# Performance work log

Measured on AMD Instinct MI355X. Metric: run time of the kernel, lower is better.

The kernel has to match this reference:

```python
import jax, jax.numpy as jnp
import numpy as np

DIM = 512; HEADS = 8; DHEAD = 64; INNER = HEADS * DHEAD
T = 9; H = 16; W = 16; KS = 5; KT = 7
SEQ = T * H * W + 1          # 2305 tokens incl. BOS
GH = 48; GW = 48             # axial grid: sqrt(T*H*W) = 48
B = 2


def _nearby_mask_np():
    """Faithful numpy port of generate_nearby_mask(causal=True). True = masked."""
    te = (KT - 1) // 2
    frame = H * W
    S = T * frame
    pad = KS // 2
    tmpl = (np.arange(KS * KS) >= (KS * KS) // 2).reshape(KS, KS)
    mb = np.ones((S, T, H + 2 * pad, W + 2 * pad), dtype=bool)
    for t in range(T):
        for h in range(H):
            for w in range(W):
                i = t * frame + h * W + w
                mb[i, t, h:h + KS, w:w + KS] = tmpl
                mb[i, max(0, t - te):t, h:h + KS, w:w + KS] = False
    mb = mb[:, :, pad:-pad, pad:-pad].reshape(S, S)
    mb = np.roll(mb, -1, axis=0)
    out = np.ones((S + 1, S + 1), dtype=bool)  # pad 1 row/col of True at top-left
    out[1:, 1:] = mb
    out[0, 0] = False
    return out


def setup_inputs() -> dict:
    key = jax.random.key(0)
    ks = jax.random.split(key, 16)
    inp = {
        "x": jax.random.normal(ks[0], (B, SEQ, DIM), jnp.float32),
        "nearby_mask": jnp.asarray(_nearby_mask_np()),
    }
    i = 1
    for l in range(3):
        for nm in ("Wq", "Wk", "Wv", "Wo"):
            inp[f"{nm}{l}"] = jax.random.normal(ks[i], (DIM, INNER), jnp.float32) * 0.02
            i += 1
        inp[f"bo{l}"] = jnp.zeros((DIM,), jnp.float32)
    return inp


def _neg(dt):
    return -jnp.finfo(dt).max


def _axial(x, Wq, Wk, Wv, Wo, bo, typ):
    # type 0: attend along rows (width axis); type 1: attend along columns.
    b = x.shape[0]
    scale = DHEAD ** -0.5
    q, k, v = x @ Wq, x @ Wk, x @ Wv

    def split(t):
        bos = t[:, :1].reshape(b, 1, HEADS, DHEAD).transpose(0, 2, 1, 3)[:, :, None]  # b hd 1 1 d
        img = t[:, 1:].reshape(b, GH, GW, HEADS, DHEAD)
        if typ == 0:
            img = img.transpose(0, 3, 1, 2, 4)  # b hd h w d
            nq = GH
        else:
            img = img.transpose(0, 3, 2, 1, 4)  # b hd w h d
            nq = GW
        bos = jnp.broadcast_to(bos, (b, HEADS, nq, 1, DHEAD))
        return jnp.concatenate([bos, img], axis=3)  # b hd nq (1+len) d

    qs, ks, vs = split(q), split(k), split(v)
    dots = jnp.einsum('bhnid,bhnjd->bhnij', qs, ks) * scale
    L = dots.shape[-1]
    causal = jnp.triu(jnp.ones((L, L), dtype=bool), 1)
    dots = jnp.where(causal, _neg(dots.dtype), dots)
    attn = jax.nn.softmax(dots, axis=-1)
    out = jnp.einsum('bhnij,bhnjd->bhnid', attn, vs)
    out_bos = out[:, :, 0, 0].reshape(b, 1, INNER)
    oi = out[:, :, :, 1:, :]
    if typ == 0:
        oi = oi.transpose(0, 2, 3, 1, 4).reshape(b, GH * GW, INNER)  # b (h w) (hd d)
    else:
        oi = oi.transpose(0, 3, 2, 1, 4).reshape(b, GH * GW, INNER)
    return jnp.concatenate([out_bos, oi], axis=1) @ Wo + bo


def _nearby(x, Wq, Wk, Wv, Wo, bo, mask):
    b, n, _ = x.shape
    scale = DHEAD ** -0.5
    q = (x @ Wq).reshape(b, n, HEADS, DHEAD).transpose(0, 2, 1, 3)
    k = (x @ Wk).reshape(b, n, HEADS, DHEAD).transpose(0, 2, 1, 3)
    v = (x @ Wv).reshape(b, n, HEADS, DHEAD).transpose(0, 2, 1, 3)
    dots = jnp.einsum('bhid,bhjd->bhij', q, k) * scale
    dots = jnp.where(mask, _neg(dots.dtype), dots)
    attn = jax.nn.softmax(dots, axis=-1)
    out = jnp.einsum('bhij,bhjd->bhid', attn, v)
    return out.transpose(0, 2, 1, 3).reshape(b, n, INNER) @ Wo + bo


def reference(x, nearby_mask,
              Wq0, Wk0, Wv0, Wo0, bo0,
              Wq1, Wk1, Wv1, Wo1, bo1,
              Wq2, Wk2, Wv2, Wo2, bo2):
    x = x + _axial(x, Wq0, Wk0, Wv0, Wo0, bo0, 0)   # row axial
    x = x + _axial(x, Wq1, Wk1, Wv1, Wo1, bo1, 1)   # column axial
    x = x + _nearby(x, Wq2, Wk2, Wv2, Wo2, bo2, nearby_mask)  # nearby sparse-mask attn
    return x
```

## Files before the change

kernel.cpp:

```cpp
#include <hip/hip_runtime.h>
#include <hip/hip_bf16.h>

#define SEQ 2305
#define NROWS 4610
#define MPAD 4736
#define DIM 512
#define QKVN 1536

typedef __attribute__((ext_vector_type(8))) short v8s;
typedef __attribute__((ext_vector_type(4))) float v4f;

__device__ __forceinline__ float bf2f(unsigned short u) {
    return __uint_as_float(((unsigned)u) << 16);
}

__device__ __forceinline__ void load_lds16(const void* g, void* l) {
    __builtin_amdgcn_global_load_lds(
        (const __attribute__((address_space(1))) void*)g,
        (__attribute__((address_space(3))) void*)l, 16, 0, 0);
}

__global__ void copy_cast(const float4* __restrict__ in, float4* __restrict__ out,
                          __hip_bfloat16* __restrict__ outb, int n4) {
    int i = blockIdx.x * blockDim.x + threadIdx.x;
    if (i >= n4) return;
    float4 v = in[i];
    out[i] = v;
    int j = i * 4;
    outb[j + 0] = __float2bfloat16(v.x);
    outb[j + 1] = __float2bfloat16(v.y);
    outb[j + 2] = __float2bfloat16(v.z);
    outb[j + 3] = __float2bfloat16(v.w);
}

struct WPack { const float* p[12]; };

__global__ void transpose_weights(WPack wp, __hip_bfloat16* __restrict__ wqkv,
                                  __hip_bfloat16* __restrict__ wo) {
    __shared__ float tile[32][33];
    int m = blockIdx.z;
    const float* src = wp.p[m];
    int l = m >> 2, j = m & 3;
    __hip_bfloat16* dst = (j < 3) ? (wqkv + (size_t)l * QKVN * DIM + (size_t)j * DIM * DIM)
                                  : (wo + (size_t)l * DIM * DIM);
    int bx = blockIdx.x * 32, by = blockIdx.y * 32;
    int tx = threadIdx.x, ty = threadIdx.y;
    #pragma unroll
    for (int i = 0; i < 4; i++)
        tile[ty + 8 * i][tx] = src[(size_t)(by + ty + 8 * i) * DIM + bx + tx];
    __syncthreads();
    #pragma unroll
    for (int i = 0; i < 4; i++)
        dst[(size_t)(bx + ty + 8 * i) * DIM + by + tx] = __float2bfloat16(tile[tx][ty + 8 * i]);
}

__global__ __launch_bounds__(256) void gemm_lds(
    const __hip_bfloat16* __restrict__ A, const __hip_bfloat16* __restrict__ Bt,
    float* __restrict__ C, const float* __restrict__ bias, const float* __restrict__ res,
    __hip_bfloat16* __restrict__ Cb, int M, int N) {
    __shared__ short As[64 * 32];
    __shared__ short Bs[128 * 32];
    const int K = 512;
    int tid = threadIdx.x;
    int wid = tid >> 6, lane = tid & 63;
    int quad = lane >> 4, l16 = lane & 15;
    int bM = blockIdx.x * 64, bN = blockIdx.y * 128;
    int wM = (wid >> 1) * 32, wN = (wid & 1) * 64;

    const short* Ag = (const short*)A;
    const short* Bg = (const short*)Bt;

    int rowS = tid >> 2, cg = tid & 3;
    const short* gA0 = Ag + (size_t)(bM + rowS) * K + cg * 8;
    const short* gB0 = Bg + (size_t)(bN + rowS) * K + cg * 8;
    const short* gB1 = Bg + (size_t)(bN + 64 + rowS) * K + cg * 8;
    short* lA0 = As + wid * 512;
    short* lB0 = Bs + wid * 512;
    short* lB1 = Bs + 2048 + wid * 512;

    v4f acc[2][4] = {};
    for (int k0 = 0; k0 < K; k0 += 32) {
        load_lds16(gA0 + k0, lA0);
        load_lds16(gB0 + k0, lB0);
        load_lds16(gB1 + k0, lB1);
        __syncthreads();
        v8s af[2], bf[4];
        #pragma unroll
        for (int i = 0; i < 2; i++)
            af[i] = *(const v8s*)(As + (wM + i * 16 + l16) * 32 + quad * 8);
        #pragma unroll
        for (int j = 0; j < 4; j++)
            bf[j] = *(const v8s*)(Bs + (wN + j * 16 + l16) * 32 + quad * 8);
        #pragma unroll
        for (int i = 0; i < 2; i++)
            #pragma unroll
            for (int j = 0; j < 4; j++)
                acc[i][j] = __builtin_amdgcn_mfma_f32_16x16x32_bf16(af[i], bf[j], acc[i][j], 0, 0, 0);
        __syncthreads();
    }

    #pragma unroll
    for (int i = 0; i < 2; i++) {
        int row = bM + wM + i * 16 + quad * 4;
        #pragma unroll
        for (int j = 0; j < 4; j++) {
            int col = bN + wN + j * 16 + l16;
            #pragma unroll
            for (int r = 0; r < 4; r++) {
                int rr = row + r;
                if (rr < M) {
                    float v = acc[i][j][r];
                    if (bias) v += bias[col];
                    if (res) v += res[(size_t)rr * N + col];
                    size_t idx = (size_t)rr * N + col;
                    if (C) C[idx] = v;
                    if (Cb) Cb[idx] = __float2bfloat16(v);
                }
            }
        }
    }
}

__global__ __launch_bounds__(256) void axial_flash(
    const unsigned short* __restrict__ qkvb, __hip_bfloat16* __restrict__ attn_b, int typ) {
    __shared__ short Ks[64 * 64];
    __shared__ short Vs[64 * 64];
    __shared__ short Ps[64 * 72];
    __shared__ float invl[64];

    int tid = threadIdx.x;
    int wid = tid >> 6, lane = tid & 63;
    int quad = lane >> 4, l16 = lane & 15;
    int n = blockIdx.x;
    int b = blockIdx.y >> 3, h = blockIdx.y & 7;
    size_t rowbase = (size_t)b * SEQ;
    int hoff = h * 64;

    #pragma unroll
    for (int it = 0; it < 2; it++) {
        int linear = it * 256 + tid;
        int slot = linear >> 3;
        int cd = linear & 7;
        int cs = cd ^ (slot & 7);
        int sp = (slot == 0) ? 0
               : (slot <= 48 ? (typ == 0 ? 1 + n * 48 + (slot - 1) : 1 + (slot - 1) * 48 + n) : 0);
        const unsigned short* srcK = qkvb + (rowbase + sp) * QKVN + hoff + 512 + cs * 8;
        load_lds16(srcK, Ks + it * 2048 + wid * 512 + lane * 8);
        const unsigned short* srcV = qkvb + (rowbase + sp) * QKVN + hoff + 1024 + cd * 8;
        load_lds16(srcV, Vs + it * 2048 + wid * 512 + lane * 8);
    }

    int qi = wid * 16 + l16;
    int sp_q = (qi >= 1 && qi <= 48)
             ? (typ == 0 ? 1 + n * 48 + (qi - 1) : 1 + (qi - 1) * 48 + n) : 0;
    const unsigned short* qptr = qkvb + (rowbase + sp_q) * QKVN + hoff + quad * 8;
    v8s qa0 = *(const v8s*)qptr;
    v8s qa1 = *(const v8s*)(qptr + 32);

    __syncthreads();

    if (n == 0 && tid < 64) {
        attn_b[rowbase * DIM + hoff + tid] =
            __float2bfloat16(bf2f(qkvb[rowbase * QKVN + hoff + 1024 + tid]));
    }

    v4f st[4];
    #pragma unroll
    for (int kt = 0; kt < 4; kt++) {
        int slot = kt * 16 + l16;
        int s7 = slot & 7;
        v8s blo = *(const v8s*)(Ks + slot * 64 + ((quad ^ s7) * 8));
        v8s bhi = *(const v8s*)(Ks + slot * 64 + (((4 + quad) ^ s7) * 8));
        v4f a = {};
        a = __builtin_amdgcn_mfma_f32_16x16x32_bf16(qa0, blo, a, 0, 0, 0);
        a = __builtin_amdgcn_mfma_f32_16x16x32_bf16(qa1, bhi, a, 0, 0, 0);
        st[kt] = a;
    }

    const float NEG = -3.0e38f;
    float sv[4][4];
    float pm[4] = {NEG, NEG, NEG, NEG};
    #pragma unroll
    for (int kt = 0; kt < 4; kt++) {
        int j = kt * 16 + l16;
        #pragma unroll
        for (int r = 0; r < 4; r++) {
            int i = wid * 16 + quad * 4 + r;
            bool ok = (i >= 1) && (i <= 48) && (j <= i);
            float v = ok ? st[kt][r] * 0.125f : NEG;
            sv[kt][r] = v;
            pm[r] = fmaxf(pm[r], v);
        }
    }
    #pragma unroll
    for (int r = 0; r < 4; r++)
        for (int o = 1; o < 16; o <<= 1) pm[r] = fmaxf(pm[r], __shfl_xor(pm[r], o));

    float ps[4] = {0.f, 0.f, 0.f, 0.f};
    #pragma unroll
    for (int kt = 0; kt < 4; kt++) {
        int j = kt * 16 + l16;
        #pragma unroll
        for (int r = 0; r < 4; r++) {
            float e = __expf(sv[kt][r] - pm[r]);
            ps[r] += e;
            Ps[(wid * 16 + quad * 4 + r) * 72 + j] = (short)__bfloat16_as_ushort(__float2bfloat16(e));
        }
    }
    #pragma unroll
    for (int r = 0; r < 4; r++)
        for (int o = 1; o < 16; o <<= 1) ps[r] += __shfl_xor(ps[r], o);
    if (l16 == 0) {
        #pragma unroll
        for (int r = 0; r < 4; r++)
            invl[wid * 16 + quad * 4 + r] = 1.0f / ps[r];
    }
    __syncthreads();

    #pragma unroll
    for (int qt = 0; qt < 4; qt++) {
        v4f oc = {};
        #pragma unroll
        for (int kc = 0; kc < 2; kc++) {
            v8s pa = *(const v8s*)(Ps + (qt * 16 + l16) * 72 + kc * 32 + quad * 8);
            v8s bfr;
            #pragma unroll
            for (int jj = 0; jj < 8; jj++)
                bfr[jj] = Vs[(kc * 32 + quad * 8 + jj) * 64 + wid * 16 + l16];
            oc = __builtin_amdgcn_mfma_f32_16x16x32_bf16(pa, bfr, oc, 0, 0, 0);
        }
        #pragma unroll
        for (int r = 0; r < 4; r++) {
            int i = qt * 16 + quad * 4 + r;
            if (i >= 1 && i <= 48) {
                int sp = typ == 0 ? 1 + n * 48 + (i - 1) : 1 + (i - 1) * 48 + n;
                attn_b[(rowbase + sp) * DIM + hoff + wid * 16 + l16] =
                    __float2bfloat16(oc[r] * invl[i]);
            }
        }
    }
}

__global__ void meanv_part(const unsigned short* __restrict__ qkvb, float* __restrict__ part) {
    int b = blockIdx.x >> 4, ch = blockIdx.x & 15;
    int col = blockIdx.y * 256 + threadIdx.x;
    int j0 = ch * 145, j1 = j0 + 145;
    if (j1 > SEQ) j1 = SEQ;
    const unsigned short* p = qkvb + (size_t)b * SEQ * QKVN + 1024 + col;
    float s = 0.f;
    #pragma unroll 4
    for (int j = j0; j < j1; j++) s += bf2f(p[(size_t)j * QKVN]);
    part[((size_t)(b * 16 + ch)) * 512 + col] = s;
}
__global__ void meanv_fold(const float* __restrict__ part,
                           const unsigned short* __restrict__ qkvb,
                           __hip_bfloat16* __restrict__ attn_b) {
    int b = blockIdx.x;
    int col = blockIdx.y * 256 + threadIdx.x;
    float s = 0.f;
    #pragma unroll
    for (int ch = 0; ch < 16; ch++) s += part[((size_t)(b * 16 + ch)) * 512 + col];
    attn_b[((size_t)b * SEQ + 2304) * DIM + col] = __float2bfloat16(s * (1.0f / 2305.0f));
    attn_b[((size_t)b * SEQ) * DIM + col] =
        __float2bfloat16(bf2f(qkvb[(size_t)b * SEQ * QKVN + 1024 + col]));
}

__global__ __launch_bounds__(256) void nearby_flash(
    const unsigned short* __restrict__ qkvb, __hip_bfloat16* __restrict__ attn_b) {
    __shared__ short KV[256 * 64];
    __shared__ __hip_bfloat16 Ps[16 * 264];
    __shared__ float redm[16 * 4];
    __shared__ float reds[16 * 4];

    int tid = threadIdx.x;
    int wid = tid >> 6, lane = tid & 63;
    int quad = lane >> 4, l16 = lane & 15;

    int idx = blockIdx.x;
    int bh = idx & 15;
    int tile = idx >> 4;
    int b = bh >> 3, h = bh & 7;
    int t = tile >> 4;
    int sxy = tile & 15;
    int hh0 = (sxy >> 2) * 4, ww0 = (sxy & 3) * 4;
    int nf = (t < 3 ? t : 3) + 1;
    int t0 = t - (nf - 1);

    size_t rowbase = (size_t)b * SEQ;
    int hoff = h * 64;

    #pragma unroll
    for (int it = 0; it < 8; it++) {
        int linear = it * 256 + tid;
        int slot = linear >> 3;
        int cd = linear & 7;
        int cs = cd ^ (slot & 7);
        int f = slot >> 6, uy = (slot >> 3) & 7, ux = slot & 7;
        int kh = hh0 - 2 + uy, kw = ww0 - 2 + ux;
        int kt = t0 + f;
        bool ok = (kh >= 0) && (kh < 16) && (kw >= 0) && (kw < 16) && (f < nf);
        int kp = ok ? (kt * 256 + kh * 16 + kw + 1) : 0;
        const unsigned short* src = qkvb + (rowbase + kp) * QKVN + hoff + 512 + cs * 8;
        load_lds16(src, KV + it * 2048 + wid * 512 + lane * 8);
    }

    int qp_f = t * 256 + (hh0 + (l16 >> 2)) * 16 + (ww0 + (l16 & 3));
    const unsigned short* qptr = qkvb + (rowbase + qp_f) * QKVN + hoff + quad * 8;
    v8s qa0 = *(const v8s*)qptr;
    v8s qa1 = *(const v8s*)(qptr + 32);

    __syncthreads();

    v4f st[4];
    #pragma unroll
    for (int k = 0; k < 4; k++) {
        int slot = (wid * 4 + k) * 16 + l16;
        int s7 = slot & 7;
        v8s blo = *(const v8s*)(KV + slot * 64 + ((quad ^ s7) * 8));
        v8s bhi = *(const v8s*)(KV + slot * 64 + (((4 + quad) ^ s7) * 8));
        v4f a = {};
        a = __builtin_amdgcn_mfma_f32_16x16x32_bf16(qa0, blo, a, 0, 0, 0);
        a = __builtin_amdgcn_mfma_f32_16x16x32_bf16(qa1, bhi, a, 0, 0, 0);
        st[k] = a;
    }

    const float NEG = -3.0e38f;
    float sv[4][4];
    float pm[4] = {NEG, NEG, NEG, NEG};
    #pragma unroll
    for (int k = 0; k < 4; k++) {
        int slot = (wid * 4 + k) * 16 + l16;
        int f = slot >> 6, uy = (slot >> 3) & 7, ux = slot & 7;
        int kh = hh0 - 2 + uy, kw = ww0 - 2 + ux;
        bool okb = (kh >= 0) && (kh < 16) && (kw >= 0) && (kw < 16) && (f < nf);
        int dyp2 = uy - quad;
        bool oky = okb && (dyp2 >= 0) && (dyp2 <= 4);
        #pragma unroll
        for (int r = 0; r < 4; r++) {
            int dxp2 = ux - r;
            bool ok = oky && (dxp2 >= 0) && (dxp2 <= 4);
            if (f == nf - 1) ok = ok && (dyp2 * 5 + dxp2 < 12);
            float v = ok ? st[k][r] * 0.125f : NEG;
            sv[k][r] = v;
            pm[r] = fmaxf(pm[r], v);
        }
    }
    #pragma unroll
    for (int r = 0; r < 4; r++)
        for (int o = 1; o < 16; o <<= 1) pm[r] = fmaxf(pm[r], __shfl_xor(pm[r], o));
    if (l16 == 0) {
        #pragma unroll
        for (int r = 0; r < 4; r++) redm[(quad * 4 + r) * 4 + wid] = pm[r];
    }
    __syncthreads();

    #pragma unroll
    for (int it = 0; it < 8; it++) {
        int linear = it * 256 + tid;
        int slot = linear >> 3;
        int cd = linear & 7;
        int f = slot >> 6, uy = (slot >> 3) & 7, ux = slot & 7;
        int kh = hh0 - 2 + uy, kw = ww0 - 2 + ux;
        int kt = t0 + f;
        bool ok = (kh >= 0) && (kh < 16) && (kw >= 0) && (kw < 16) && (f < nf);
        int kp = ok ? (kt * 256 + kh * 16 + kw + 1) : 0;
        const unsigned short* src = qkvb + (rowbase + kp) * QKVN + hoff + 1024 + cd * 8;
        load_lds16(src, KV + it * 2048 + wid * 512 + lane * 8);
    }

    float rm[4];
    #pragma unroll
    for (int r = 0; r < 4; r++) {
        int row = (quad * 4 + r) * 4;
        rm[r] = fmaxf(fmaxf(redm[row], redm[row + 1]), fmaxf(redm[row + 2], redm[row + 3]));
    }

    float ps[4] = {0.f, 0.f, 0.f, 0.f};
    #pragma unroll
    for (int k = 0; k < 4; k++) {
        int slot = (wid * 4 + k) * 16 + l16;
        #pragma unroll
        for (int r = 0; r < 4; r++) {
            float e = __expf(sv[k][r] - rm[r]);
            ps[r] += e;
            Ps[(quad * 4 + r) * 264 + slot] = __float2bfloat16(e);
        }
    }
    #pragma unroll
    for (int r = 0; r < 4; r++)
        for (int o = 1; o < 16; o <<= 1) ps[r] += __shfl_xor(ps[r], o);
    if (l16 == 0) {
        #pragma unroll
        for (int r = 0; r < 4; r++) reds[(quad * 4 + r) * 4 + wid] = ps[r];
    }
    __syncthreads();

    float inv[4];
    #pragma unroll
    for (int r = 0; r < 4; r++) {
        int row = (quad * 4 + r) * 4;
        float d = reds[row] + reds[row + 1] + reds[row + 2] + reds[row + 3];
        inv[r] = 1.0f / d;
    }

    v4f oc = {};
    #pragma unroll
    for (int kc = 0; kc < 8; kc++) {
        v8s pa = *(const v8s*)((const short*)Ps + l16 * 264 + kc * 32 + quad * 8);
        v8s bf;
        #pragma unroll
        for (int j = 0; j < 8; j++) {
            int slot = kc * 32 + quad * 8 + j;
            bf[j] = KV[slot * 64 + wid * 16 + l16];
        }
        oc = __builtin_amdgcn_mfma_f32_16x16x32_bf16(pa, bf, oc, 0, 0, 0);
    }

    #pragma unroll
    for (int r = 0; r < 4; r++) {
        int qp = t * 256 + (hh0 + quad) * 16 + (ww0 + r);
        if (qp != 0) {
            attn_b[(rowbase + qp) * DIM + hoff + wid * 16 + l16] =
                __float2bfloat16(oc[r] * inv[r]);
        }
    }
}

extern "C" void kernel_launch(void* const* d_in, const int* in_sizes, int n_in,
                              void* d_out, int out_size, void* d_ws, size_t ws_size,
                              hipStream_t stream) {
    const float* x = (const float*)d_in[0];
    float* xcur = (float*)d_out;

    char* ws = (char*)d_ws;
    size_t off = 0;
    auto alloc = [&](size_t bytes) -> void* {
        void* p = ws + off;
        off = (off + bytes + 255) & ~(size_t)255;
        return p;
    };
    __hip_bfloat16* wqkv  = (__hip_bfloat16*)alloc((size_t)3 * QKVN * DIM * 2);
    __hip_bfloat16* wo    = (__hip_bfloat16*)alloc((size_t)3 * DIM * DIM * 2);
    __hip_bfloat16* xb    = (__hip_bfloat16*)alloc((size_t)MPAD * DIM * 2);
    __hip_bfloat16* attnb = (__hip_bfloat16*)alloc((size_t)MPAD * DIM * 2);
    float* part           = (float*)alloc((size_t)2 * 16 * 512 * 4);
    __hip_bfloat16* qkvb  = (__hip_bfloat16*)alloc((size_t)NROWS * QKVN * 2);

    const int nElem = NROWS * DIM;
    const int n4 = nElem / 4;

    copy_cast<<<(n4 + 255) / 256, 256, 0, stream>>>((const float4*)x, (float4*)xcur, xb, n4);

    WPack wp;
    for (int l = 0; l < 3; l++)
        for (int j = 0; j < 4; j++)
            wp.p[l * 4 + j] = (const float*)d_in[2 + l * 5 + j];
    transpose_weights<<<dim3(16, 16, 12), dim3(32, 8), 0, stream>>>(wp, wqkv, wo);

    for (int l = 0; l < 3; l++) {
        gemm_lds<<<dim3(MPAD / 64, QKVN / 128), 256, 0, stream>>>(
            xb, wqkv + (size_t)l * QKVN * DIM, nullptr, nullptr, nullptr, qkvb, NROWS, QKVN);
        if (l < 2) {
            axial_flash<<<dim3(48, 16), 256, 0, stream>>>((const unsigned short*)qkvb, attnb, l);
        } else {
            meanv_part<<<dim3(32, 2), 256, 0, stream>>>((const unsigned short*)qkvb, part);
            meanv_fold<<<dim3(2, 2), 256, 0, stream>>>(part, (const unsigned short*)qkvb, attnb);
            nearby_flash<<<2304, 256, 0, stream>>>((const unsigned short*)qkvb, attnb);
        }
        const float* bo = (const float*)d_in[6 + l * 5];
        gemm_lds<<<dim3(MPAD / 64, DIM / 128), 256, 0, stream>>>(
            attnb, wo + (size_t)l * DIM * DIM, xcur, bo, xcur, xb, NROWS, DIM);
    }
}
```

Measured before the change: 296.9 us.

## Fuse prep kernels, fold mean-V into nearby attention, double K-step in GEMM

Merges the input copy/cast into the weight-transpose launch as an extra z-slice, and moves the mean-of-V reduction for the BOS and last rows into 16 extra blocks of the nearby attention kernel. This drops three small kernel launches. The GEMM now loads two 32-wide K slices per barrier pair, halving the synchronisations at the cost of twice the shared memory. The mean-V blocks each reduce 2305 strided rows alone, so they may become stragglers at the end of the attention launch.

```diff
diff --git a/kernel.cpp b/kernel.cpp
--- a/kernel.cpp
+++ b/kernel.cpp
@@ -20,31 +20,34 @@
         (__attribute__((address_space(3))) void*)l, 16, 0, 0);
 }
 
-__global__ void copy_cast(const float4* __restrict__ in, float4* __restrict__ out,
-                          __hip_bfloat16* __restrict__ outb, int n4) {
-    int i = blockIdx.x * blockDim.x + threadIdx.x;
-    if (i >= n4) return;
-    float4 v = in[i];
-    out[i] = v;
-    int j = i * 4;
-    outb[j + 0] = __float2bfloat16(v.x);
-    outb[j + 1] = __float2bfloat16(v.y);
-    outb[j + 2] = __float2bfloat16(v.z);
-    outb[j + 3] = __float2bfloat16(v.w);
-}
-
 struct WPack { const float* p[12]; };
 
-__global__ void transpose_weights(WPack wp, __hip_bfloat16* __restrict__ wqkv,
-                                  __hip_bfloat16* __restrict__ wo) {
+__global__ void prep_inputs(WPack wp, __hip_bfloat16* __restrict__ wqkv,
+                            __hip_bfloat16* __restrict__ wo,
+                            const float4* __restrict__ xin, float4* __restrict__ xout,
+                            __hip_bfloat16* __restrict__ xb, int n4) {
+    int tx = threadIdx.x, ty = threadIdx.y;
+    int m = blockIdx.z;
+    if (m == 12) {
+        int tidl = ty * 32 + tx;
+        int bid = blockIdx.y * 16 + blockIdx.x;
+        for (int i = bid * 256 + tidl; i < n4; i += 65536) {
+            float4 v = xin[i];
+            xout[i] = v;
+            int j = i * 4;
+            xb[j + 0] = __float2bfloat16(v.x);
+            xb[j + 1] = __float2bfloat16(v.y);
+            xb[j + 2] = __float2bfloat16(v.z);
+            xb[j + 3] = __float2bfloat16(v.w);
+        }
+        return;
+    }
     __shared__ float tile[32][33];
-    int m = blockIdx.z;
     const float* src = wp.p[m];
     int l = m >> 2, j = m & 3;
     __hip_bfloat16* dst = (j < 3) ? (wqkv + (size_t)l * QKVN * DIM + (size_t)j * DIM * DIM)
                                   : (wo + (size_t)l * DIM * DIM);
     int bx = blockIdx.x * 32, by = blockIdx.y * 32;
-    int tx = threadIdx.x, ty = threadIdx.y;
     #pragma unroll
     for (int i = 0; i < 4; i++)
         tile[ty + 8 * i][tx] = src[(size_t)(by + ty + 8 * i) * DIM + bx + tx];
@@ -58,8 +61,8 @@
     const __hip_bfloat16* __restrict__ A, const __hip_bfloat16* __restrict__ Bt,
     float* __restrict__ C, const float* __restrict__ bias, const float* __restrict__ res,
     __hip_bfloat16* __restrict__ Cb, int M, int N) {
-    __shared__ short As[64 * 32];
-    __shared__ short Bs[128 * 32];
+    __shared__ short As[2][64 * 32];
+    __shared__ short Bs[2][128 * 32];
     const int K = 512;
     int tid = threadIdx.x;
     int wid = tid >> 6, lane = tid & 63;
@@ -71,31 +74,34 @@
     const short* Bg = (const short*)Bt;
 
     int rowS = tid >> 2, cg = tid & 3;
-    const short* gA0 = Ag + (size_t)(bM + rowS) * K + cg * 8;
+    const short* gA = Ag + (size_t)(bM + rowS) * K + cg * 8;
     const short* gB0 = Bg + (size_t)(bN + rowS) * K + cg * 8;
     const short* gB1 = Bg + (size_t)(bN + 64 + rowS) * K + cg * 8;
-    short* lA0 = As + wid * 512;
-    short* lB0 = Bs + wid * 512;
-    short* lB1 = Bs + 2048 + wid * 512;
 
     v4f acc[2][4] = {};
-    for (int k0 = 0; k0 < K; k0 += 32) {
-        load_lds16(gA0 + k0, lA0);
-        load_lds16(gB0 + k0, lB0);
-        load_lds16(gB1 + k0, lB1);
+    for (int k0 = 0; k0 < K; k0 += 64) {
+        #pragma unroll
+        for (int s = 0; s < 2; s++) {
+            load_lds16(gA + k0 + s * 32, As[s] + wid * 512);
+            load_lds16(gB0 + k0 + s * 32, Bs[s] + wid * 512);
+            load_lds16(gB1 + k0 + s * 32, Bs[s] + 2048 + wid * 512);
+        }
         __syncthreads();
-        v8s af[2], bf[4];
-        #pragma unroll
-        for (int i = 0; i < 2; i++)
-            af[i] = *(const v8s*)(As + (wM + i * 16 + l16) * 32 + quad * 8);
-        #pragma unroll
-        for (int j = 0; j < 4; j++)
-            bf[j] = *(const v8s*)(Bs + (wN + j * 16 + l16) * 32 + quad * 8);
-        #pragma unroll
-        for (int i = 0; i < 2; i++)
+        #pragma unroll
+        for (int s = 0; s < 2; s++) {
+            v8s af[2], bf[4];
+            #pragma unroll
+            for (int i = 0; i < 2; i++)
+                af[i] = *(const v8s*)(As[s] + (wM + i * 16 + l16) * 32 + quad * 8);
             #pragma unroll
             for (int j = 0; j < 4; j++)
-                acc[i][j] = __builtin_amdgcn_mfma_f32_16x16x32_bf16(af[i], bf[j], acc[i][j], 0, 0, 0);
+                bf[j] = *(const v8s*)(Bs[s] + (wN + j * 16 + l16) * 32 + quad * 8);
+            #pragma unroll
+            for (int i = 0; i < 2; i++)
+                #pragma unroll
+                for (int j = 0; j < 4; j++)
+                    acc[i][j] = __builtin_amdgcn_mfma_f32_16x16x32_bf16(af[i], bf[j], acc[i][j], 0, 0, 0);
+        }
         __syncthreads();
     }
 
@@ -241,30 +247,6 @@
     }
 }
 
-__global__ void meanv_part(const unsigned short* __restrict__ qkvb, float* __restrict__ part) {
-    int b = blockIdx.x >> 4, ch = blockIdx.x & 15;
-    int col = blockIdx.y * 256 + threadIdx.x;
-    int j0 = ch * 145, j1 = j0 + 145;
-    if (j1 > SEQ) j1 = SEQ;
-    const unsigned short* p = qkvb + (size_t)b * SEQ * QKVN + 1024 + col;
-    float s = 0.f;
-    #pragma unroll 4
-    for (int j = j0; j < j1; j++) s += bf2f(p[(size_t)j * QKVN]);
-    part[((size_t)(b * 16 + ch)) * 512 + col] = s;
-}
-__global__ void meanv_fold(const float* __restrict__ part,
-                           const unsigned short* __restrict__ qkvb,
-                           __hip_bfloat16* __restrict__ attn_b) {
-    int b = blockIdx.x;
-    int col = blockIdx.y * 256 + threadIdx.x;
-    float s = 0.f;
-    #pragma unroll
-    for (int ch = 0; ch < 16; ch++) s += part[((size_t)(b * 16 + ch)) * 512 + col];
-    attn_b[((size_t)b * SEQ + 2304) * DIM + col] = __float2bfloat16(s * (1.0f / 2305.0f));
-    attn_b[((size_t)b * SEQ) * DIM + col] =
-        __float2bfloat16(bf2f(qkvb[(size_t)b * SEQ * QKVN + 1024 + col]));
-}
-
 __global__ __launch_bounds__(256) void nearby_flash(
     const unsigned short* __restrict__ qkvb, __hip_bfloat16* __restrict__ attn_b) {
     __shared__ short KV[256 * 64];
@@ -277,6 +259,31 @@
     int quad = lane >> 4, l16 = lane & 15;
 
     int idx = blockIdx.x;
+    if (idx >= 2304) {
+        int bh = idx - 2304;
+        int b = bh >> 3, h = bh & 7;
+        size_t rb = (size_t)b * SEQ;
+        const unsigned short* vb = qkvb + rb * QKVN + h * 64 + 1024 + lane;
+        float s0 = 0.f, s1 = 0.f, s2 = 0.f, s3 = 0.f;
+        int j = wid;
+        for (; j + 12 < SEQ; j += 16) {
+            s0 += bf2f(vb[(size_t)j * QKVN]);
+            s1 += bf2f(vb[(size_t)(j + 4) * QKVN]);
+            s2 += bf2f(vb[(size_t)(j + 8) * QKVN]);
+            s3 += bf2f(vb[(size_t)(j + 12) * QKVN]);
+        }
+        for (; j < SEQ; j += 4) s0 += bf2f(vb[(size_t)j * QKVN]);
+        float* red = (float*)KV;
+        red[wid * 64 + lane] = s0 + s1 + s2 + s3;
+        __syncthreads();
+        if (wid == 0) {
+            float tot = red[lane] + red[64 + lane] + red[128 + lane] + red[192 + lane];
+            attn_b[(rb + 2304) * DIM + h * 64 + lane] = __float2bfloat16(tot * (1.0f / 2305.0f));
+            attn_b[rb * DIM + h * 64 + lane] = __float2bfloat16(bf2f(vb[0]));
+        }
+        return;
+    }
+
     int bh = idx & 15;
     int tile = idx >> 4;
     int b = bh >> 3, h = bh & 7;
@@ -443,19 +450,17 @@
     __hip_bfloat16* wo    = (__hip_bfloat16*)alloc((size_t)3 * DIM * DIM * 2);
     __hip_bfloat16* xb    = (__hip_bfloat16*)alloc((size_t)MPAD * DIM * 2);
     __hip_bfloat16* attnb = (__hip_bfloat16*)alloc((size_t)MPAD * DIM * 2);
-    float* part           = (float*)alloc((size_t)2 * 16 * 512 * 4);
     __hip_bfloat16* qkvb  = (__hip_bfloat16*)alloc((size_t)NROWS * QKVN * 2);
 
     const int nElem = NROWS * DIM;
     const int n4 = nElem / 4;
-
-    copy_cast<<<(n4 + 255) / 256, 256, 0, stream>>>((const float4*)x, (float4*)xcur, xb, n4);
 
     WPack wp;
     for (int l = 0; l < 3; l++)
         for (int j = 0; j < 4; j++)
             wp.p[l * 4 + j] = (const float*)d_in[2 + l * 5 + j];
-    transpose_weights<<<dim3(16, 16, 12), dim3(32, 8), 0, stream>>>(wp, wqkv, wo);
+    prep_inputs<<<dim3(16, 16, 13), dim3(32, 8), 0, stream>>>(
+        wp, wqkv, wo, (const float4*)x, (float4*)xcur, xb, n4);
 
     for (int l = 0; l < 3; l++) {
         gemm_lds<<<dim3(MPAD / 64, QKVN / 128), 256, 0, stream>>>(
@@ -463,9 +468,7 @@
         if (l < 2) {
             axial_flash<<<dim3(48, 16), 256, 0, stream>>>((const unsigned short*)qkvb, attnb, l);
         } else {
-            meanv_part<<<dim3(32, 2), 256, 0, stream>>>((const unsigned short*)qkvb, part);
-            meanv_fold<<<dim3(2, 2), 256, 0, stream>>>(part, (const unsigned short*)qkvb, attnb);
-            nearby_flash<<<2304, 256, 0, stream>>>((const unsigned short*)qkvb, attnb);
+            nearby_flash<<<2304 + 16, 256, 0, stream>>>((const unsigned short*)qkvb, attnb);
         }
         const float* bo = (const float*)d_in[6 + l * 5];
         gemm_lds<<<dim3(MPAD / 64, DIM / 128), 256, 0, stream>>>(
```

Measured after the change: 295.2 us. About the same (-0.6%).
